# Performance work log

Measured on AMD Instinct MI355X. Metric: run time of the kernel, lower is better.

## Reference

```python
import jax, jax.numpy as jnp
import numpy as np

B, TE, TD, H, N_HIDDEN = 8, 4096, 1024, 256, 256

def setup_inputs() -> dict:
    key = jax.random.key(0)
    k_e, k_d, k_w, k_b = jax.random.split(key, 4)
    e = jax.random.normal(k_e, (B, TE, H), dtype=jnp.float32)
    d = jax.random.normal(k_d, (B, TD, H), dtype=jnp.float32)
    # Dense(n_hidden, activation='tanh') params: kernel [2H, n_hidden], bias [n_hidden]
    W = jax.random.normal(k_w, (2 * H, N_HIDDEN), dtype=jnp.float32) * (1.0 / np.sqrt(2 * H))
    b = jnp.zeros((N_HIDDEN,), dtype=jnp.float32)
    return {"e": e, "d": d, "W": W, "b": b}

def reference(e, d, W, b):
    # scores: Dot(axes=(2,2)) -> [B, Td, Te]
    scores = jnp.einsum('bth,bsh->bts', d, e)
    attn = jax.nn.softmax(scores, axis=-1)
    # value: Dot(axes=(2,1)) -> [B, Td, H]
    value = jnp.einsum('bts,bsh->bth', attn, e)
    concat = jnp.concatenate([value, d], axis=-1)  # [B, Td, 2H]
    return jnp.tanh(concat @ W + b)  # [B, Td, n_hidden]
```

## Files before the change

### kernel.cpp

```cpp
#include <hip/hip_runtime.h>


#define B_ 8
#define TE_ 4096
#define TD_ 1024
#define H_ 256
#define NS_ 4
#define CHUNK_ (TE_ / NS_)
#define NIT_ (CHUNK_ / 32)
#define NROW_ (B_ * TD_)

typedef __attribute__((ext_vector_type(8))) short s16x8;
typedef __attribute__((ext_vector_type(8))) _Float16 h16x8;
typedef __attribute__((ext_vector_type(4))) float fx4;
typedef __attribute__((ext_vector_type(16))) float fx16;
typedef __attribute__((ext_vector_type(4))) unsigned short u16x4;

__device__ __forceinline__ h16x8 as_h(s16x8 v) {
  union { s16x8 s; h16x8 h; } u; u.s = v; return u.h;
}
#define MFMA(a, b, c) __builtin_amdgcn_mfma_f32_16x16x32_f16(as_h(a), as_h(b), c, 0, 0, 0)
#define MFMA32(a, b, c) __builtin_amdgcn_mfma_f32_32x32x16_f16(as_h(a), as_h(b), c, 0, 0, 0)

__device__ __forceinline__ unsigned short f2h(float x) {
  const _Float16 h = (_Float16)x;
  union { _Float16 h; unsigned short s; } u; u.h = h; return u.s;
}
__device__ __forceinline__ float h2f(unsigned short s) {
  union { unsigned short s; _Float16 h; } u; u.s = s; return (float)u.h;
}
__device__ __forceinline__ unsigned pk2h(float f0, float f1) {
  return (unsigned)f2h(f0) | ((unsigned)f2h(f1) << 16);
}
__device__ __forceinline__ void gload_lds16(const void* g, void* l) {
  __builtin_amdgcn_global_load_lds(
      (const __attribute__((address_space(1))) void*)g,
      (__attribute__((address_space(3))) void*)l, 16, 0, 0);
}

__global__ __launch_bounds__(256) void prep(const float* __restrict__ e,
                                            const float* __restrict__ W,
                                            unsigned short* __restrict__ eh,
                                            unsigned short* __restrict__ eT,
                                            unsigned short* __restrict__ WT) {
  __shared__ unsigned short lt[64][65];
  __shared__ float wl[32][33];
  const int bid = blockIdx.x;
  const int tid = threadIdx.x;
  if (bid < 2048) {
    const int b = bid >> 8;
    const int s0 = ((bid >> 2) & 63) * 64;
    const int h0 = (bid & 3) * 64;
#pragma unroll
    for (int i = 0; i < 4; ++i) {
      const int row = (tid >> 4) + 16 * i;
      const int col = (tid & 15) * 4;
      const size_t go = (((size_t)b * TE_) + s0 + row) * H_ + h0 + col;
      const fx4 v = *(const fx4*)&e[go];
      u16x4 hv;
#pragma unroll
      for (int j = 0; j < 4; ++j) {
        const unsigned short hb = f2h(v[j]);
        hv[j] = hb;
        lt[row][col + j] = hb;
      }
      *(u16x4*)&eh[go] = hv;
    }
    __syncthreads();
#pragma unroll
    for (int i = 0; i < 2; ++i) {
      const int idx = tid + 256 * i;
      const int hh = idx >> 3;
      const int sc = (idx & 7) * 8;
      s16x8 v;
#pragma unroll
      for (int j = 0; j < 8; ++j) v[j] = (short)lt[sc + j][hh];
      *(s16x8*)&eT[(((size_t)b * H_) + h0 + hh) * TE_ + s0 + sc] = v;
    }
  } else {
    const int tb = bid - 2048;
    const int k0 = (tb >> 3) * 32, n0 = (tb & 7) * 32;
    const int r = tid >> 3, c4 = (tid & 7) * 4;
    const fx4 v = *(const fx4*)&W[(size_t)(k0 + r) * 256 + n0 + c4];
#pragma unroll
    for (int j = 0; j < 4; ++j) wl[r][c4 + j] = v[j];
    __syncthreads();
    u16x4 o;
#pragma unroll
    for (int j = 0; j < 4; ++j) o[j] = f2h(wl[c4 + j][r]);
    *(u16x4*)&WT[(size_t)(n0 + r) * 512 + k0 + c4] = o;
  }
}

__global__ __launch_bounds__(512, 2) void flash16(
    const unsigned short* __restrict__ eh_g, const unsigned short* __restrict__ eT_g,
    const float* __restrict__ dmat,
    unsigned short* __restrict__ pacc, float* __restrict__ pm,
    float* __restrict__ pl) {
  const int bid = blockIdx.x;
  const int ns = bid & 3;
  const int qb = (bid >> 2) & 7;
  const int b = bid >> 5;
  const int tid = threadIdx.x;
  const int w = tid >> 6;
  const int lane = tid & 63;
  const int g = lane >> 4, c = lane & 15;
  const int qrow = qb * 128 + w * 16 + c;

  __shared__ uint4 smem[4][2][1024];

  const unsigned short *peh0, *peh1, *pet0, *pet1;
  {
    const size_t ebase = ((size_t)b * TE_ + ns * CHUNK_) * H_;
    const size_t tbase = (size_t)b * H_ * TE_ + ns * CHUNK_;
    int L = tid;
    int s = L >> 5, ch = L & 31;
    int sg = (s & 3) | (((s >> 3) & 1) << 2);
    peh0 = eh_g + ebase + s * H_ + (ch ^ sg) * 8;
    int h2 = (L >> 6) * 16 + (L & 15), sc = ((L >> 4) & 3) * 8;
    pet0 = eT_g + tbase + (size_t)h2 * TE_ + sc;
    L = tid + 512;
    s = L >> 5; ch = L & 31;
    sg = (s & 3) | (((s >> 3) & 1) << 2);
    peh1 = eh_g + ebase + s * H_ + (ch ^ sg) * 8;
    h2 = (L >> 6) * 16 + (L & 15); sc = ((L >> 4) & 3) * 8;
    pet1 = eT_g + tbase + (size_t)h2 * TE_ + sc;
  }
  auto STAGE = [&](int buf) {
    uint4* ehb = smem[buf][0];
    uint4* etb = smem[buf][1];
    gload_lds16(peh0, &ehb[tid]);
    gload_lds16(peh1, &ehb[tid + 512]);
    gload_lds16(pet0, &etb[tid]);
    gload_lds16(pet1, &etb[tid + 512]);
    peh0 += 32 * H_; peh1 += 32 * H_;
    pet0 += 32; pet1 += 32;
  };

  STAGE(0);
  STAGE(1);

  s16x8 bd_h[8], bd_l[8];
  {
    const float* dr = dmat + ((size_t)b * TD_ + qrow) * H_;
#pragma unroll
    for (int kk = 0; kk < 8; ++kk) {
      const fx4 x0 = *(const fx4*)&dr[kk * 32 + g * 8];
      const fx4 x1 = *(const fx4*)&dr[kk * 32 + g * 8 + 4];
      s16x8 hh, ll;
#pragma unroll
      for (int j = 0; j < 4; ++j) {
        unsigned short hb = f2h(x0[j]);
        hh[j] = (short)hb; ll[j] = (short)f2h(x0[j] - h2f(hb));
        hb = f2h(x1[j]);
        hh[4 + j] = (short)hb; ll[4 + j] = (short)f2h(x1[j] - h2f(hb));
      }
      bd_h[kk] = hh; bd_l[kk] = ll;
    }
  }

  fx4 acc[16];
#pragma unroll
  for (int nt = 0; nt < 16; ++nt) acc[nt] = (fx4){0.f, 0.f, 0.f, 0.f};
  float m = -__builtin_inff(), l_lane = 0.f;
  const int xr = (c & 3) | (((c >> 2) & 1) << 2);
  const int rho = (c & 3) + (c >> 2) * 8;

  __syncthreads();

  for (int p = 0; p < NIT_ / 2; ++p) {
    const int bufA = (p & 1) << 1;
    const int bufB = bufA + 1;
    if (p + 1 < NIT_ / 2) {
      STAGE(bufA ^ 2);
      STAGE(bufB ^ 2);
    }
    const uint4* ehbA = smem[bufA][0];
    const uint4* etbA = smem[bufA][1];
    const uint4* ehbB = smem[bufB][0];
    const uint4* etbB = smem[bufB][1];

    fx4 sA0 = (fx4){0.f, 0.f, 0.f, 0.f};
    fx4 sA1 = (fx4){0.f, 0.f, 0.f, 0.f};
    fx4 sB0 = (fx4){0.f, 0.f, 0.f, 0.f};
    fx4 sB1 = (fx4){0.f, 0.f, 0.f, 0.f};
#pragma unroll
    for (int kk = 0; kk < 8; ++kk) {
      const int sl = (kk * 4 + g) ^ xr;
      const s16x8 aA0 = *(const s16x8*)&ehbA[rho * 32 + sl];
      const s16x8 aA1 = *(const s16x8*)&ehbA[(rho + 4) * 32 + sl];
      const s16x8 aB0 = *(const s16x8*)&ehbB[rho * 32 + sl];
      const s16x8 aB1 = *(const s16x8*)&ehbB[(rho + 4) * 32 + sl];
      sA0 = MFMA(aA0, bd_h[kk], sA0);
      sA0 = MFMA(aA0, bd_l[kk], sA0);
      sA1 = MFMA(aA1, bd_h[kk], sA1);
      sA1 = MFMA(aA1, bd_l[kk], sA1);
      sB0 = MFMA(aB0, bd_h[kk], sB0);
      sB0 = MFMA(aB0, bd_l[kk], sB0);
      sB1 = MFMA(aB1, bd_h[kk], sB1);
      sB1 = MFMA(aB1, bd_l[kk], sB1);
    }

    float mx = fmaxf(fmaxf(fmaxf(sA0[0], sA0[1]), fmaxf(sA0[2], sA0[3])),
                     fmaxf(fmaxf(sA1[0], sA1[1]), fmaxf(sA1[2], sA1[3])));
    mx = fmaxf(mx, fmaxf(fmaxf(fmaxf(sB0[0], sB0[1]), fmaxf(sB0[2], sB0[3])),
                         fmaxf(fmaxf(sB1[0], sB1[1]), fmaxf(sB1[2], sB1[3]))));
    mx = fmaxf(mx, __shfl_xor(mx, 16, 64));
    mx = fmaxf(mx, __shfl_xor(mx, 32, 64));
    if (!__all(mx <= m + 4.0f)) {
      const float nm = fmaxf(m, mx);
      const float sc = __expf(m - nm);
      m = nm; l_lane *= sc;
#pragma unroll
      for (int nt = 0; nt < 16; ++nt) {
#pragma unroll
        for (int r = 0; r < 4; ++r) acc[nt][r] *= sc;
      }
    }

    {
      float t0[4], t1[4];
#pragma unroll
      for (int r = 0; r < 4; ++r) {
        t0[r] = __expf(sA0[r] - m);
        t1[r] = __expf(sA1[r] - m);
        l_lane += t0[r] + t1[r];
      }
      union { unsigned u[4]; s16x8 v; } pb;
      pb.u[0] = pk2h(t0[0], t0[1]);
      pb.u[1] = pk2h(t0[2], t0[3]);
      pb.u[2] = pk2h(t1[0], t1[1]);
      pb.u[3] = pk2h(t1[2], t1[3]);
#pragma unroll
      for (int nt = 0; nt < 16; ++nt) {
        const s16x8 ea = *(const s16x8*)&etbA[nt * 64 + g * 16 + c];
        acc[nt] = MFMA(ea, pb.v, acc[nt]);
      }
    }
    {
      float t0[4], t1[4];
#pragma unroll
      for (int r = 0; r < 4; ++r) {
        t0[r] = __expf(sB0[r] - m);
        t1[r] = __expf(sB1[r] - m);
        l_lane += t0[r] + t1[r];
      }
      union { unsigned u[4]; s16x8 v; } pb;
      pb.u[0] = pk2h(t0[0], t0[1]);
      pb.u[1] = pk2h(t0[2], t0[3]);
      pb.u[2] = pk2h(t1[0], t1[1]);
      pb.u[3] = pk2h(t1[2], t1[3]);
#pragma unroll
      for (int nt = 0; nt < 16; ++nt) {
        const s16x8 ea = *(const s16x8*)&etbB[nt * 64 + g * 16 + c];
        acc[nt] = MFMA(ea, pb.v, acc[nt]);
      }
    }
    __syncthreads();
  }

  float l = l_lane;
  l += __shfl_xor(l, 16, 64);
  l += __shfl_xor(l, 32, 64);

  const size_t R = (size_t)b * TD_ + qrow;
  unsigned short* pr = pacc + (((size_t)ns * NROW_) + R) * H_;
#pragma unroll
  for (int nt = 0; nt < 16; ++nt) {
    u16x4 o;
#pragma unroll
    for (int j = 0; j < 4; ++j) o[j] = f2h(acc[nt][j]);
    *(u16x4*)(pr + nt * 16 + g * 4) = o;
  }
  if (g == 0) {
    pm[ns * NROW_ + R] = m;
    pl[ns * NROW_ + R] = l;
  }
}

__global__ __launch_bounds__(256) void dense2(const unsigned short* __restrict__ pacc,
                                              const float* __restrict__ pm,
                                              const float* __restrict__ pl,
                                              const float* __restrict__ dmat,
                                              const unsigned short* __restrict__ WT,
                                              const float* __restrict__ bias,
                                              float* __restrict__ out) {
  const int row0 = blockIdx.x * 32;
  const int tid = threadIdx.x;
  const int w = tid >> 6;
  const int lane = tid & 63;
  const int ln = lane & 31, hi = lane >> 5;
  __shared__ unsigned short Xl[32][520];

  {
    const int row = tid >> 3;
    const int c0 = (tid & 7) * 32;
    const int R = row0 + row;
    float wts[NS_];
    float M = -__builtin_inff();
#pragma unroll
    for (int s = 0; s < NS_; ++s) M = fmaxf(M, pm[s * NROW_ + R]);
    float L = 0.f;
#pragma unroll
    for (int s = 0; s < NS_; ++s) {
      wts[s] = __expf(pm[s * NROW_ + R] - M);
      L += wts[s] * pl[s * NROW_ + R];
    }
    const float inv = 1.0f / L;
#pragma unroll
    for (int c8 = 0; c8 < 4; ++c8) {
      const int cc = c0 + c8 * 8;
      float o8[8];
#pragma unroll
      for (int j = 0; j < 8; ++j) o8[j] = 0.f;
#pragma unroll
      for (int s = 0; s < NS_; ++s) {
        const s16x8 v = *(const s16x8*)&pacc[(((size_t)s * NROW_) + R) * H_ + cc];
#pragma unroll
        for (int j = 0; j < 8; ++j)
          o8[j] += wts[s] * h2f((unsigned short)v[j]);
      }
      u16x4 y0, y1;
#pragma unroll
      for (int j = 0; j < 4; ++j) {
        y0[j] = f2h(o8[j] * inv);
        y1[j] = f2h(o8[4 + j] * inv);
      }
      *(u16x4*)&Xl[row][cc] = y0;
      *(u16x4*)&Xl[row][cc + 4] = y1;
    }
    const float* drow = dmat + (size_t)R * H_ + c0;
#pragma unroll
    for (int c8 = 0; c8 < 8; ++c8) {
      const fx4 v = *(const fx4*)&drow[c8 * 4];
      u16x4 y;
#pragma unroll
      for (int j = 0; j < 4; ++j) y[j] = f2h(v[j]);
      *(u16x4*)&Xl[row][256 + c0 + c8 * 4] = y;
    }
  }
  __syncthreads();

  fx16 a0, a1;
#pragma unroll
  for (int r = 0; r < 16; ++r) { a0[r] = 0.f; a1[r] = 0.f; }
  const int n0 = w * 64;
#pragma unroll
  for (int ks = 0; ks < 32; ++ks) {
    const s16x8 av = *(const s16x8*)&Xl[ln][ks * 16 + hi * 8];
    const s16x8 b0 = *(const s16x8*)(WT + (size_t)(n0 + ln) * 512 + ks * 16 + hi * 8);
    const s16x8 b1 = *(const s16x8*)(WT + (size_t)(n0 + 32 + ln) * 512 + ks * 16 + hi * 8);
    a0 = MFMA32(av, b0, a0);
    a1 = MFMA32(av, b1, a1);
  }
  const float bn0 = bias[n0 + ln];
  const float bn1 = bias[n0 + 32 + ln];
#pragma unroll
  for (int r = 0; r < 16; ++r) {
    const int rloc = (r & 3) + 8 * (r >> 2) + 4 * hi;
    const size_t ro = (size_t)(row0 + rloc) * 256;
    out[ro + n0 + ln] = tanhf(a0[r] + bn0);
    out[ro + n0 + 32 + ln] = tanhf(a1[r] + bn1);
  }
}

extern "C" void kernel_launch(void* const* d_in, const int* in_sizes, int n_in,
                              void* d_out, int out_size, void* d_ws, size_t ws_size,
                              hipStream_t stream) {
  const float* e = (const float*)d_in[0];
  const float* d = (const float*)d_in[1];
  const float* W = (const float*)d_in[2];
  const float* bias = (const float*)d_in[3];
  float* out = (float*)d_out;

  char* p = (char*)d_ws;
  const size_t EB = (size_t)B_ * TE_ * H_ * 2;
  const size_t WB = (size_t)512 * 256 * 2;
  const size_t PB = (size_t)NS_ * NROW_ * H_ * 2;
  unsigned short* eh  = (unsigned short*)p;            p += EB;
  unsigned short* eT  = (unsigned short*)p;            p += EB;
  unsigned short* WT  = (unsigned short*)p;            p += WB;
  unsigned short* pacc = (unsigned short*)p;           p += PB;
  float* pmv = (float*)p;                              p += (size_t)NS_ * NROW_ * 4;
  float* plv = (float*)p;

  prep<<<dim3(2176), dim3(256), 0, stream>>>(e, W, eh, eT, WT);
  flash16<<<dim3(256), dim3(512), 0, stream>>>(eh, eT, d, pacc, pmv, plv);
  dense2<<<dim3(256), dim3(256), 0, stream>>>(pacc, pmv, plv, d, WT, bias, out);
}
```

Baseline: 92.67 us.

## Process two query row groups per wave in flash kernel with 256-thread blocks

The flash attention kernel now runs 4 waves per block instead of 8, and each wave handles 32 query rows (two 16-row groups) instead of 16. Each LDS fragment of e and eT is therefore reused for twice as many MFMAs, which halves LDS read traffic per unit of compute. Each thread now holds twice the accumulators and query fragments, so register pressure rises. With launch_bounds(256,1) and the same 128KB of shared memory per block, there are fewer waves per CU to hide latency.

After: 112.8 us. +21.7%, slower.

```diff
diff --git a/kernel.cpp b/kernel.cpp
--- a/kernel.cpp
+++ b/kernel.cpp
@@ -92,7 +92,7 @@
   }
 }
 
-__global__ __launch_bounds__(512, 2) void flash16(
+__global__ __launch_bounds__(256, 1) void flash18(
     const unsigned short* __restrict__ eh_g, const unsigned short* __restrict__ eT_g,
     const float* __restrict__ dmat,
     unsigned short* __restrict__ pacc, float* __restrict__ pm,
@@ -105,44 +105,45 @@
   const int w = tid >> 6;
   const int lane = tid & 63;
   const int g = lane >> 4, c = lane & 15;
-  const int qrow = qb * 128 + w * 16 + c;
+  const int qrow0 = qb * 128 + w * 32 + c;
+  const int qrow1 = qrow0 + 16;
 
   __shared__ uint4 smem[4][2][1024];
 
-  const unsigned short *peh0, *peh1, *pet0, *pet1;
+  const unsigned short* pEh[4];
+  const unsigned short* pEt[4];
   {
     const size_t ebase = ((size_t)b * TE_ + ns * CHUNK_) * H_;
     const size_t tbase = (size_t)b * H_ * TE_ + ns * CHUNK_;
-    int L = tid;
-    int s = L >> 5, ch = L & 31;
-    int sg = (s & 3) | (((s >> 3) & 1) << 2);
-    peh0 = eh_g + ebase + s * H_ + (ch ^ sg) * 8;
-    int h2 = (L >> 6) * 16 + (L & 15), sc = ((L >> 4) & 3) * 8;
-    pet0 = eT_g + tbase + (size_t)h2 * TE_ + sc;
-    L = tid + 512;
-    s = L >> 5; ch = L & 31;
-    sg = (s & 3) | (((s >> 3) & 1) << 2);
-    peh1 = eh_g + ebase + s * H_ + (ch ^ sg) * 8;
-    h2 = (L >> 6) * 16 + (L & 15); sc = ((L >> 4) & 3) * 8;
-    pet1 = eT_g + tbase + (size_t)h2 * TE_ + sc;
+#pragma unroll
+    for (int i = 0; i < 4; ++i) {
+      const int L = tid + 256 * i;
+      const int s = L >> 5, ch = L & 31;
+      const int sg = (s & 3) | (((s >> 3) & 1) << 2);
+      pEh[i] = eh_g + ebase + s * H_ + (ch ^ sg) * 8;
+      const int h2 = (L >> 6) * 16 + (L & 15), sc = ((L >> 4) & 3) * 8;
+      pEt[i] = eT_g + tbase + (size_t)h2 * TE_ + sc;
+    }
   }
   auto STAGE = [&](int buf) {
     uint4* ehb = smem[buf][0];
     uint4* etb = smem[buf][1];
-    gload_lds16(peh0, &ehb[tid]);
-    gload_lds16(peh1, &ehb[tid + 512]);
-    gload_lds16(pet0, &etb[tid]);
-    gload_lds16(pet1, &etb[tid + 512]);
-    peh0 += 32 * H_; peh1 += 32 * H_;
-    pet0 += 32; pet1 += 32;
+#pragma unroll
+    for (int i = 0; i < 4; ++i) {
+      gload_lds16(pEh[i], &ehb[tid + 256 * i]);
+      gload_lds16(pEt[i], &etb[tid + 256 * i]);
+      pEh[i] += 32 * H_;
+      pEt[i] += 32;
+    }
   };
 
   STAGE(0);
   STAGE(1);
 
-  s16x8 bd_h[8], bd_l[8];
-  {
-    const float* dr = dmat + ((size_t)b * TD_ + qrow) * H_;
+  s16x8 bd_h[2][8], bd_l[2][8];
+#pragma unroll
+  for (int grp = 0; grp < 2; ++grp) {
+    const float* dr = dmat + ((size_t)b * TD_ + (grp ? qrow1 : qrow0)) * H_;
 #pragma unroll
     for (int kk = 0; kk < 8; ++kk) {
       const fx4 x0 = *(const fx4*)&dr[kk * 32 + g * 8];
@@ -155,14 +156,18 @@
         hb = f2h(x1[j]);
         hh[4 + j] = (short)hb; ll[4 + j] = (short)f2h(x1[j] - h2f(hb));
       }
-      bd_h[kk] = hh; bd_l[kk] = ll;
-    }
-  }
-
-  fx4 acc[16];
-#pragma unroll
-  for (int nt = 0; nt < 16; ++nt) acc[nt] = (fx4){0.f, 0.f, 0.f, 0.f};
-  float m = -__builtin_inff(), l_lane = 0.f;
+      bd_h[grp][kk] = hh; bd_l[grp][kk] = ll;
+    }
+  }
+
+  fx4 acc0[16], acc1[16];
+#pragma unroll
+  for (int nt = 0; nt < 16; ++nt) {
+    acc0[nt] = (fx4){0.f, 0.f, 0.f, 0.f};
+    acc1[nt] = (fx4){0.f, 0.f, 0.f, 0.f};
+  }
+  float m0 = -__builtin_inff(), m1 = -__builtin_inff();
+  float l0 = 0.f, l1 = 0.f;
   const int xr = (c & 3) | (((c >> 2) & 1) << 2);
   const int rho = (c & 3) + (c >> 2) * 8;
 
@@ -180,10 +185,10 @@
     const uint4* ehbB = smem[bufB][0];
     const uint4* etbB = smem[bufB][1];
 
-    fx4 sA0 = (fx4){0.f, 0.f, 0.f, 0.f};
-    fx4 sA1 = (fx4){0.f, 0.f, 0.f, 0.f};
-    fx4 sB0 = (fx4){0.f, 0.f, 0.f, 0.f};
-    fx4 sB1 = (fx4){0.f, 0.f, 0.f, 0.f};
+    fx4 sA0g0 = (fx4){0.f,0.f,0.f,0.f}, sA1g0 = (fx4){0.f,0.f,0.f,0.f};
+    fx4 sB0g0 = (fx4){0.f,0.f,0.f,0.f}, sB1g0 = (fx4){0.f,0.f,0.f,0.f};
+    fx4 sA0g1 = (fx4){0.f,0.f,0.f,0.f}, sA1g1 = (fx4){0.f,0.f,0.f,0.f};
+    fx4 sB0g1 = (fx4){0.f,0.f,0.f,0.f}, sB1g1 = (fx4){0.f,0.f,0.f,0.f};
 #pragma unroll
     for (int kk = 0; kk < 8; ++kk) {
       const int sl = (kk * 4 + g) ^ xr;
@@ -191,90 +196,131 @@
       const s16x8 aA1 = *(const s16x8*)&ehbA[(rho + 4) * 32 + sl];
       const s16x8 aB0 = *(const s16x8*)&ehbB[rho * 32 + sl];
       const s16x8 aB1 = *(const s16x8*)&ehbB[(rho + 4) * 32 + sl];
-      sA0 = MFMA(aA0, bd_h[kk], sA0);
-      sA0 = MFMA(aA0, bd_l[kk], sA0);
-      sA1 = MFMA(aA1, bd_h[kk], sA1);
-      sA1 = MFMA(aA1, bd_l[kk], sA1);
-      sB0 = MFMA(aB0, bd_h[kk], sB0);
-      sB0 = MFMA(aB0, bd_l[kk], sB0);
-      sB1 = MFMA(aB1, bd_h[kk], sB1);
-      sB1 = MFMA(aB1, bd_l[kk], sB1);
-    }
-
-    float mx = fmaxf(fmaxf(fmaxf(sA0[0], sA0[1]), fmaxf(sA0[2], sA0[3])),
-                     fmaxf(fmaxf(sA1[0], sA1[1]), fmaxf(sA1[2], sA1[3])));
-    mx = fmaxf(mx, fmaxf(fmaxf(fmaxf(sB0[0], sB0[1]), fmaxf(sB0[2], sB0[3])),
-                         fmaxf(fmaxf(sB1[0], sB1[1]), fmaxf(sB1[2], sB1[3]))));
-    mx = fmaxf(mx, __shfl_xor(mx, 16, 64));
-    mx = fmaxf(mx, __shfl_xor(mx, 32, 64));
-    if (!__all(mx <= m + 4.0f)) {
-      const float nm = fmaxf(m, mx);
-      const float sc = __expf(m - nm);
-      m = nm; l_lane *= sc;
+      sA0g0 = MFMA(aA0, bd_h[0][kk], sA0g0);
+      sA0g0 = MFMA(aA0, bd_l[0][kk], sA0g0);
+      sA0g1 = MFMA(aA0, bd_h[1][kk], sA0g1);
+      sA0g1 = MFMA(aA0, bd_l[1][kk], sA0g1);
+      sA1g0 = MFMA(aA1, bd_h[0][kk], sA1g0);
+      sA1g0 = MFMA(aA1, bd_l[0][kk], sA1g0);
+      sA1g1 = MFMA(aA1, bd_h[1][kk], sA1g1);
+      sA1g1 = MFMA(aA1, bd_l[1][kk], sA1g1);
+      sB0g0 = MFMA(aB0, bd_h[0][kk], sB0g0);
+      sB0g0 = MFMA(aB0, bd_l[0][kk], sB0g0);
+      sB0g1 = MFMA(aB0, bd_h[1][kk], sB0g1);
+      sB0g1 = MFMA(aB0, bd_l[1][kk], sB0g1);
+      sB1g0 = MFMA(aB1, bd_h[0][kk], sB1g0);
+      sB1g0 = MFMA(aB1, bd_l[0][kk], sB1g0);
+      sB1g1 = MFMA(aB1, bd_h[1][kk], sB1g1);
+      sB1g1 = MFMA(aB1, bd_l[1][kk], sB1g1);
+    }
+
+    float mx0 = fmaxf(fmaxf(fmaxf(sA0g0[0], sA0g0[1]), fmaxf(sA0g0[2], sA0g0[3])),
+                      fmaxf(fmaxf(sA1g0[0], sA1g0[1]), fmaxf(sA1g0[2], sA1g0[3])));
+    mx0 = fmaxf(mx0, fmaxf(fmaxf(fmaxf(sB0g0[0], sB0g0[1]), fmaxf(sB0g0[2], sB0g0[3])),
+                           fmaxf(fmaxf(sB1g0[0], sB1g0[1]), fmaxf(sB1g0[2], sB1g0[3]))));
+    float mx1 = fmaxf(fmaxf(fmaxf(sA0g1[0], sA0g1[1]), fmaxf(sA0g1[2], sA0g1[3])),
+                      fmaxf(fmaxf(sA1g1[0], sA1g1[1]), fmaxf(sA1g1[2], sA1g1[3])));
+    mx1 = fmaxf(mx1, fmaxf(fmaxf(fmaxf(sB0g1[0], sB0g1[1]), fmaxf(sB0g1[2], sB0g1[3])),
+                           fmaxf(fmaxf(sB1g1[0], sB1g1[1]), fmaxf(sB1g1[2], sB1g1[3]))));
+    mx0 = fmaxf(mx0, __shfl_xor(mx0, 16, 64));
+    mx0 = fmaxf(mx0, __shfl_xor(mx0, 32, 64));
+    mx1 = fmaxf(mx1, __shfl_xor(mx1, 16, 64));
+    mx1 = fmaxf(mx1, __shfl_xor(mx1, 32, 64));
+    const bool ok = (mx0 <= m0 + 4.0f) && (mx1 <= m1 + 4.0f);
+    if (!__all(ok)) {
+      const float nm0 = fmaxf(m0, mx0);
+      const float sc0 = __expf(m0 - nm0);
+      const float nm1 = fmaxf(m1, mx1);
+      const float sc1 = __expf(m1 - nm1);
+      m0 = nm0; m1 = nm1; l0 *= sc0; l1 *= sc1;
 #pragma unroll
       for (int nt = 0; nt < 16; ++nt) {
 #pragma unroll
-        for (int r = 0; r < 4; ++r) acc[nt][r] *= sc;
+        for (int r = 0; r < 4; ++r) { acc0[nt][r] *= sc0; acc1[nt][r] *= sc1; }
       }
     }
 
     {
-      float t0[4], t1[4];
-#pragma unroll
-      for (int r = 0; r < 4; ++r) {
-        t0[r] = __expf(sA0[r] - m);
-        t1[r] = __expf(sA1[r] - m);
-        l_lane += t0[r] + t1[r];
-      }
-      union { unsigned u[4]; s16x8 v; } pb;
-      pb.u[0] = pk2h(t0[0], t0[1]);
-      pb.u[1] = pk2h(t0[2], t0[3]);
-      pb.u[2] = pk2h(t1[0], t1[1]);
-      pb.u[3] = pk2h(t1[2], t1[3]);
+      union { unsigned u[4]; s16x8 v; } pb0, pb1;
+      {
+        float t0[4], t1[4];
+#pragma unroll
+        for (int r = 0; r < 4; ++r) {
+          t0[r] = __expf(sA0g0[r] - m0);
+          t1[r] = __expf(sA1g0[r] - m0);
+          l0 += t0[r] + t1[r];
+        }
+        pb0.u[0] = pk2h(t0[0], t0[1]); pb0.u[1] = pk2h(t0[2], t0[3]);
+        pb0.u[2] = pk2h(t1[0], t1[1]); pb0.u[3] = pk2h(t1[2], t1[3]);
+#pragma unroll
+        for (int r = 0; r < 4; ++r) {
+          t0[r] = __expf(sA0g1[r] - m1);
+          t1[r] = __expf(sA1g1[r] - m1);
+          l1 += t0[r] + t1[r];
+        }
+        pb1.u[0] = pk2h(t0[0], t0[1]); pb1.u[1] = pk2h(t0[2], t0[3]);
+        pb1.u[2] = pk2h(t1[0], t1[1]); pb1.u[3] = pk2h(t1[2], t1[3]);
+      }
 #pragma unroll
       for (int nt = 0; nt < 16; ++nt) {
         const s16x8 ea = *(const s16x8*)&etbA[nt * 64 + g * 16 + c];
-        acc[nt] = MFMA(ea, pb.v, acc[nt]);
+        acc0[nt] = MFMA(ea, pb0.v, acc0[nt]);
+        acc1[nt] = MFMA(ea, pb1.v, acc1[nt]);
       }
     }
     {
-      float t0[4], t1[4];
-#pragma unroll
-      for (int r = 0; r < 4; ++r) {
-        t0[r] = __expf(sB0[r] - m);
-        t1[r] = __expf(sB1[r] - m);
-        l_lane += t0[r] + t1[r];
-      }
-      union { unsigned u[4]; s16x8 v; } pb;
-      pb.u[0] = pk2h(t0[0], t0[1]);
-      pb.u[1] = pk2h(t0[2], t0[3]);
-      pb.u[2] = pk2h(t1[0], t1[1]);
-      pb.u[3] = pk2h(t1[2], t1[3]);
+      union { unsigned u[4]; s16x8 v; } pb0, pb1;
+      {
+        float t0[4], t1[4];
+#pragma unroll
+        for (int r = 0; r < 4; ++r) {
+          t0[r] = __expf(sB0g0[r] - m0);
+          t1[r] = __expf(sB1g0[r] - m0);
+          l0 += t0[r] + t1[r];
+        }
+        pb0.u[0] = pk2h(t0[0], t0[1]); pb0.u[1] = pk2h(t0[2], t0[3]);
+        pb0.u[2] = pk2h(t1[0], t1[1]); pb0.u[3] = pk2h(t1[2], t1[3]);
+#pragma unroll
+        for (int r = 0; r < 4; ++r) {
+          t0[r] = __expf(sB0g1[r] - m1);
+          t1[r] = __expf(sB1g1[r] - m1);
+          l1 += t0[r] + t1[r];
+        }
+        pb1.u[0] = pk2h(t0[0], t0[1]); pb1.u[1] = pk2h(t0[2], t0[3]);
+        pb1.u[2] = pk2h(t1[0], t1[1]); pb1.u[3] = pk2h(t1[2], t1[3]);
+      }
 #pragma unroll
       for (int nt = 0; nt < 16; ++nt) {
         const s16x8 ea = *(const s16x8*)&etbB[nt * 64 + g * 16 + c];
-        acc[nt] = MFMA(ea, pb.v, acc[nt]);
+        acc0[nt] = MFMA(ea, pb0.v, acc0[nt]);
+        acc1[nt] = MFMA(ea, pb1.v, acc1[nt]);
       }
     }
     __syncthreads();
   }
 
-  float l = l_lane;
-  l += __shfl_xor(l, 16, 64);
-  l += __shfl_xor(l, 32, 64);
-
-  const size_t R = (size_t)b * TD_ + qrow;
-  unsigned short* pr = pacc + (((size_t)ns * NROW_) + R) * H_;
+  l0 += __shfl_xor(l0, 16, 64);
+  l0 += __shfl_xor(l0, 32, 64);
+  l1 += __shfl_xor(l1, 16, 64);
+  l1 += __shfl_xor(l1, 32, 64);
+
+  const size_t R0 = (size_t)b * TD_ + qrow0;
+  const size_t R1 = (size_t)b * TD_ + qrow1;
+  unsigned short* pr0 = pacc + (((size_t)ns * NROW_) + R0) * H_;
+  unsigned short* pr1 = pacc + (((size_t)ns * NROW_) + R1) * H_;
 #pragma unroll
   for (int nt = 0; nt < 16; ++nt) {
-    u16x4 o;
-#pragma unroll
-    for (int j = 0; j < 4; ++j) o[j] = f2h(acc[nt][j]);
-    *(u16x4*)(pr + nt * 16 + g * 4) = o;
+    u16x4 o0, o1;
+#pragma unroll
+    for (int j = 0; j < 4; ++j) { o0[j] = f2h(acc0[nt][j]); o1[j] = f2h(acc1[nt][j]); }
+    *(u16x4*)(pr0 + nt * 16 + g * 4) = o0;
+    *(u16x4*)(pr1 + nt * 16 + g * 4) = o1;
   }
   if (g == 0) {
-    pm[ns * NROW_ + R] = m;
-    pl[ns * NROW_ + R] = l;
+    pm[ns * NROW_ + R0] = m0;
+    pl[ns * NROW_ + R0] = l0;
+    pm[ns * NROW_ + R1] = m1;
+    pl[ns * NROW_ + R1] = l1;
   }
 }
 
@@ -385,6 +431,6 @@
   float* plv = (float*)p;
 
   prep<<<dim3(2176), dim3(256), 0, stream>>>(e, W, eh, eT, WT);
-  flash16<<<dim3(256), dim3(512), 0, stream>>>(eh, eT, d, pacc, pmv, plv);
+  flash18<<<dim3(256), dim3(256), 0, stream>>>(eh, eT, d, pacc, pmv, plv);
   dense2<<<dim3(256), dim3(256), 0, stream>>>(pacc, pmv, plv, d, WT, bias, out);
 }
```
